# Performance work log

Measured on AMD Instinct MI355X. Metric: run time of the kernel, lower is better.

## Reference

```python
import jax, jax.numpy as jnp
import numpy as np


def _chamfer(src, tgt):
    # src: [B, N, 3], tgt: [B, M, 3]
    x2 = jnp.sum(src * src, axis=-1)              # [B, N]
    y2 = jnp.sum(tgt * tgt, axis=-1)              # [B, M]
    xy = jnp.einsum('bnd,bmd->bnm', src, tgt)     # [B, N, M]
    d2 = x2[:, :, None] + y2[:, None, :] - 2.0 * xy
    d2 = jnp.maximum(d2, 0.0)                     # guard tiny negatives
    cham_x = jnp.min(d2, axis=2)                  # [B, N] min over tgt
    cham_y = jnp.min(d2, axis=1)                  # [B, M] min over src
    # point_reduction='mean', batch_reduction='sum'
    loss = jnp.sum(jnp.mean(cham_x, axis=1)) + jnp.sum(jnp.mean(cham_y, axis=1))
    return loss


def setup_inputs() -> dict:
    key = jax.random.key(0)
    k1, k2 = jax.random.split(key)
    src = jax.random.normal(k1, (16, 4096, 3), dtype=jnp.float32)
    tgt = jax.random.normal(k2, (16, 4096, 3), dtype=jnp.float32)
    return {"src": src, "tgt": tgt}


def reference(src, tgt):
    wgeo = 1.0
    return wgeo * _chamfer(src, tgt)
```

## Files before the change

### kernel.cpp

```cpp
#include <hip/hip_runtime.h>
#include <hip/hip_bf16.h>


#define BATCH   16
#define NPTS    4096
#define CHUNKC  512
#define NCHUNKS (NPTS / CHUNKC)
#define NSTRIPS 32

typedef __attribute__((ext_vector_type(8)))  short short8;
typedef __attribute__((ext_vector_type(16))) float float16;

union U4S8 { uint4 u; short8 s; };

__device__ inline unsigned int bfb(float v) {
    __hip_bfloat16 h = __float2bfloat16(v);
    unsigned short u; __builtin_memcpy(&u, &h, 2);
    return (unsigned int)u;
}
__device__ inline float bff(float v) { return __bfloat162float(__float2bfloat16(v)); }

#define ONEB 0x3F80u

__device__ inline void buildA(float x, float y, float z, uint4& w0, uint4& w1) {
    float xhf = bff(x), yhf = bff(y), zhf = bff(z);
    float f = fmaf(x, x, fmaf(y, y, z * z));
    float fhf = bff(f);
    unsigned xh = bfb(xhf), yh = bfb(yhf), zh = bfb(zhf);
    unsigned xl = bfb(x - xhf), yl = bfb(y - yhf), zl = bfb(z - zhf);
    unsigned fh = bfb(fhf), fl = bfb(f - fhf);
    w0 = make_uint4(xh | (yh << 16), zh | (xh << 16),
                    yh | (zh << 16), xl | (yl << 16));
    w1 = make_uint4(zl | (fh << 16), fl | (ONEB << 16), ONEB, 0u);
}

__device__ inline void buildB(float x, float y, float z, uint4& w0, uint4& w1) {
    float xhf = bff(x), yhf = bff(y), zhf = bff(z);
    float f = fmaf(x, x, fmaf(y, y, z * z));
    float fhf = bff(f);
    unsigned a = bfb(-2.0f * xhf), b = bfb(-2.0f * yhf), c = bfb(-2.0f * zhf);
    unsigned d = bfb(-2.0f * (x - xhf)), e = bfb(-2.0f * (y - yhf)),
             g = bfb(-2.0f * (z - zhf));
    unsigned fh = bfb(fhf), fl = bfb(f - fhf);
    w0 = make_uint4(a | (b << 16), c | (d << 16),
                    e | (g << 16), a | (b << 16));
    w1 = make_uint4(c | (ONEB << 16), ONEB | (fh << 16), fl, 0u);
}

__global__ __launch_bounds__(256, 4) void chamfer_kernel(
    const float* __restrict__ src, const float* __restrict__ tgt,
    float* __restrict__ out)
{
    __shared__ uint4 sbuf[2][2][CHUNKC];
    __shared__ float wsum[4];

    int blk = blockIdx.x;
    const int strip = blk & (NSTRIPS - 1); blk >>= 5;
    const int b     = blk & 15;            blk >>= 4;
    const int dir   = blk;

    const int t    = threadIdx.x;
    const int lane = t & 63;
    const int w    = t >> 6;
    const int half = lane >> 5;
    const int l5   = lane & 31;

    const float* Araw = (dir ? tgt : src) + (size_t)b * NPTS * 3;
    const float* Braw = (dir ? src : tgt) + (size_t)b * NPTS * 3;

    short8 afr;
    {
        int row = strip * 128 + w * 32 + l5;
        uint4 w0, w1;
        buildA(Araw[3 * row], Araw[3 * row + 1], Araw[3 * row + 2], w0, w1);
        U4S8 tt; tt.u = half ? w1 : w0;
        afr = tt.s;
    }

    float nx[2][3];
    auto loadRaw = [&](int c) {
#pragma unroll
        for (int k = 0; k < 2; k++) {
            int p = c * CHUNKC + t + k * 256;
            nx[k][0] = Braw[3 * p + 0];
            nx[k][1] = Braw[3 * p + 1];
            nx[k][2] = Braw[3 * p + 2];
        }
    };
    auto convertWrite = [&](int bi) {
#pragma unroll
        for (int k = 0; k < 2; k++) {
            int lp = t + k * 256;
            uint4 w0, w1;
            buildB(nx[k][0], nx[k][1], nx[k][2], w0, w1);
            sbuf[bi][0][lp] = w0;
            sbuf[bi][1][lp] = w1;
        }
    };

    const float16 z16 = {0.f,0.f,0.f,0.f,0.f,0.f,0.f,0.f,
                         0.f,0.f,0.f,0.f,0.f,0.f,0.f,0.f};
    float rm[16];
#pragma unroll
    for (int r = 0; r < 16; r++) rm[r] = 1e30f;

    loadRaw(0);
    convertWrite(0);
    for (int c = 0; c < NCHUNKS; c++) {
        __syncthreads();
        if (c + 1 < NCHUNKS) loadRaw(c + 1);
        const int bi = c & 1;
#pragma unroll 2
        for (int j2 = 0; j2 < CHUNKC / 64; j2++) {
            U4S8 t0, t1;
            t0.u = sbuf[bi][half][j2 * 64 + l5];
            t1.u = sbuf[bi][half][j2 * 64 + 32 + l5];
            float16 a0 = __builtin_amdgcn_mfma_f32_32x32x16_bf16(afr, t0.s, z16, 0, 0, 0);
            float16 a1 = __builtin_amdgcn_mfma_f32_32x32x16_bf16(afr, t1.s, z16, 0, 0, 0);
#pragma unroll
            for (int r = 0; r < 16; r++)
                rm[r] = fminf(fminf(a0[r], a1[r]), rm[r]);
        }
        if (c + 1 < NCHUNKS) convertWrite((c + 1) & 1);
    }

#pragma unroll
    for (int mask = 1; mask <= 16; mask <<= 1)
#pragma unroll
        for (int r = 0; r < 16; r++)
            rm[r] = fminf(rm[r], __shfl_xor(rm[r], mask, 64));

    float s = 0.0f;
#pragma unroll
    for (int r = 0; r < 16; r++) s += fmaxf(rm[r], 0.0f);
    s += __shfl_xor(s, 32, 64);

    if (lane == 0) wsum[w] = s;
    __syncthreads();
    if (t == 0)
        atomicAdd(out, (wsum[0] + wsum[1] + wsum[2] + wsum[3]) * (1.0f / (float)NPTS));
}

extern "C" void kernel_launch(void* const* d_in, const int* in_sizes, int n_in,
                              void* d_out, int out_size, void* d_ws, size_t ws_size,
                              hipStream_t stream)
{
    const float* src = (const float*)d_in[0];
    const float* tgt = (const float*)d_in[1];
    float* out = (float*)d_out;

    hipMemsetAsync(out, 0, sizeof(float), stream);
    chamfer_kernel<<<2 * BATCH * NSTRIPS, 256, 0, stream>>>(src, tgt, out);
}
```

Before: 81.46 us.

## Give each wave two A row-tiles and double chunk size with LDS prefetch

Each wave now holds two 32-row A fragments, so every B fragment read from LDS feeds four MFMAs instead of two, halving LDS reads per MFMA. The number of strips per batch drops to 16, chunks grow to 1024 points, and the next step's B fragments are read ahead of the current MFMAs. In exchange, register pressure rises (two 16-float min accumulators, four staged points), launch bounds fall to 2 blocks per CU, LDS use doubles, and the grid has half as many blocks (512).

```diff
diff --git a/kernel.cpp b/kernel.cpp
--- a/kernel.cpp
+++ b/kernel.cpp
@@ -4,9 +4,10 @@
 
 #define BATCH   16
 #define NPTS    4096
-#define CHUNKC  512
+#define CHUNKC  1024
 #define NCHUNKS (NPTS / CHUNKC)
-#define NSTRIPS 32
+#define NSTRIPS 16
+#define NSTEP   (CHUNKC / 64)
 
 typedef __attribute__((ext_vector_type(8)))  short short8;
 typedef __attribute__((ext_vector_type(16))) float float16;
@@ -47,7 +48,7 @@
     w1 = make_uint4(c | (ONEB << 16), ONEB | (fh << 16), fl, 0u);
 }
 
-__global__ __launch_bounds__(256, 4) void chamfer_kernel(
+__global__ __launch_bounds__(256, 2) void chamfer_kernel(
     const float* __restrict__ src, const float* __restrict__ tgt,
     float* __restrict__ out)
 {
@@ -55,7 +56,7 @@
     __shared__ float wsum[4];
 
     int blk = blockIdx.x;
-    const int strip = blk & (NSTRIPS - 1); blk >>= 5;
+    const int strip = blk & (NSTRIPS - 1); blk >>= 4;
     const int b     = blk & 15;            blk >>= 4;
     const int dir   = blk;
 
@@ -68,19 +69,20 @@
     const float* Araw = (dir ? tgt : src) + (size_t)b * NPTS * 3;
     const float* Braw = (dir ? src : tgt) + (size_t)b * NPTS * 3;
 
-    short8 afr;
-    {
-        int row = strip * 128 + w * 32 + l5;
+    short8 afr[2];
+#pragma unroll
+    for (int g = 0; g < 2; g++) {
+        int row = strip * 256 + g * 128 + w * 32 + l5;
         uint4 w0, w1;
         buildA(Araw[3 * row], Araw[3 * row + 1], Araw[3 * row + 2], w0, w1);
         U4S8 tt; tt.u = half ? w1 : w0;
-        afr = tt.s;
+        afr[g] = tt.s;
     }
 
-    float nx[2][3];
+    float nx[4][3];
     auto loadRaw = [&](int c) {
 #pragma unroll
-        for (int k = 0; k < 2; k++) {
+        for (int k = 0; k < 4; k++) {
             int p = c * CHUNKC + t + k * 256;
             nx[k][0] = Braw[3 * p + 0];
             nx[k][1] = Braw[3 * p + 1];
@@ -89,7 +91,7 @@
     };
     auto convertWrite = [&](int bi) {
 #pragma unroll
-        for (int k = 0; k < 2; k++) {
+        for (int k = 0; k < 4; k++) {
             int lp = t + k * 256;
             uint4 w0, w1;
             buildB(nx[k][0], nx[k][1], nx[k][2], w0, w1);
@@ -100,9 +102,11 @@
 
     const float16 z16 = {0.f,0.f,0.f,0.f,0.f,0.f,0.f,0.f,
                          0.f,0.f,0.f,0.f,0.f,0.f,0.f,0.f};
-    float rm[16];
+    float rm[2][16];
 #pragma unroll
-    for (int r = 0; r < 16; r++) rm[r] = 1e30f;
+    for (int g = 0; g < 2; g++)
+#pragma unroll
+        for (int r = 0; r < 16; r++) rm[g][r] = 1e30f;
 
     loadRaw(0);
     convertWrite(0);
@@ -110,16 +114,25 @@
         __syncthreads();
         if (c + 1 < NCHUNKS) loadRaw(c + 1);
         const int bi = c & 1;
-#pragma unroll 2
-        for (int j2 = 0; j2 < CHUNKC / 64; j2++) {
-            U4S8 t0, t1;
-            t0.u = sbuf[bi][half][j2 * 64 + l5];
-            t1.u = sbuf[bi][half][j2 * 64 + 32 + l5];
-            float16 a0 = __builtin_amdgcn_mfma_f32_32x32x16_bf16(afr, t0.s, z16, 0, 0, 0);
-            float16 a1 = __builtin_amdgcn_mfma_f32_32x32x16_bf16(afr, t1.s, z16, 0, 0, 0);
+
+        U4S8 c0, c1, n0, n1;
+        c0.u = sbuf[bi][half][l5];
+        c1.u = sbuf[bi][half][32 + l5];
+#pragma unroll 4
+        for (int j2 = 0; j2 < NSTEP; j2++) {
+            int nj = (j2 + 1) & (NSTEP - 1);
+            n0.u = sbuf[bi][half][nj * 64 + l5];
+            n1.u = sbuf[bi][half][nj * 64 + 32 + l5];
+            float16 a00 = __builtin_amdgcn_mfma_f32_32x32x16_bf16(afr[0], c0.s, z16, 0, 0, 0);
+            float16 a01 = __builtin_amdgcn_mfma_f32_32x32x16_bf16(afr[0], c1.s, z16, 0, 0, 0);
+            float16 a10 = __builtin_amdgcn_mfma_f32_32x32x16_bf16(afr[1], c0.s, z16, 0, 0, 0);
+            float16 a11 = __builtin_amdgcn_mfma_f32_32x32x16_bf16(afr[1], c1.s, z16, 0, 0, 0);
 #pragma unroll
-            for (int r = 0; r < 16; r++)
-                rm[r] = fminf(fminf(a0[r], a1[r]), rm[r]);
+            for (int r = 0; r < 16; r++) {
+                rm[0][r] = fminf(fminf(a00[r], a01[r]), rm[0][r]);
+                rm[1][r] = fminf(fminf(a10[r], a11[r]), rm[1][r]);
+            }
+            c0 = n0; c1 = n1;
         }
         if (c + 1 < NCHUNKS) convertWrite((c + 1) & 1);
     }
@@ -127,12 +140,16 @@
 #pragma unroll
     for (int mask = 1; mask <= 16; mask <<= 1)
 #pragma unroll
-        for (int r = 0; r < 16; r++)
-            rm[r] = fminf(rm[r], __shfl_xor(rm[r], mask, 64));
+        for (int g = 0; g < 2; g++)
+#pragma unroll
+            for (int r = 0; r < 16; r++)
+                rm[g][r] = fminf(rm[g][r], __shfl_xor(rm[g][r], mask, 64));
 
     float s = 0.0f;
 #pragma unroll
-    for (int r = 0; r < 16; r++) s += fmaxf(rm[r], 0.0f);
+    for (int g = 0; g < 2; g++)
+#pragma unroll
+        for (int r = 0; r < 16; r++) s += fmaxf(rm[g][r], 0.0f);
     s += __shfl_xor(s, 32, 64);
 
     if (lane == 0) wsum[w] = s;
```

After: 78.11 us. 1.04x faster.
